# Kernel optimization log

Measured on AMD Instinct MI355X. Metric: run time of the kernel, lower is better.

Reference implementation:

```python
import jax, jax.numpy as jnp
import numpy as np

DIM = 2048
N_HEAD = 32
N_KV = 8
HEAD_DIM = DIM // N_HEAD  # 64
GROUP = N_HEAD // N_KV    # 4


def setup_inputs() -> dict:
    key = jax.random.key(0)
    k1, k2, k3, k4 = jax.random.split(key, 4)
    B, S = 2, 2048
    x = jax.random.normal(k1, (B, S, DIM), dtype=jnp.float32)
    freqs_cis = jax.random.normal(k2, (S, HEAD_DIM // 2, 2), dtype=jnp.float32)
    wqkv_w = jax.random.normal(k3, (DIM, (N_HEAD + 2 * N_KV) * HEAD_DIM), dtype=jnp.float32) * 0.02
    wo_w = jax.random.normal(k4, (DIM, DIM), dtype=jnp.float32) * 0.02
    return {"x": x, "freqs_cis": freqs_cis, "wqkv_w": wqkv_w, "wo_w": wo_w}


def apply_rotary_emb(x, freqs_cis):
    # x: (B, S, H, head_dim), freqs_cis: (S, head_dim//2, 2)
    B, S, H, D = x.shape
    xs = x.astype(jnp.float32).reshape(B, S, H, D // 2, 2)
    fc = freqs_cis.reshape(1, S, 1, D // 2, 2)
    real = xs[..., 0] * fc[..., 0] - xs[..., 1] * fc[..., 1]
    imag = xs[..., 1] * fc[..., 0] + xs[..., 0] * fc[..., 1]
    out = jnp.stack([real, imag], axis=-1).reshape(B, S, H, D)
    return out.astype(x.dtype)


def reference(x, freqs_cis, wqkv_w, wo_w):
    B, S, _ = x.shape
    kv_size = N_KV * HEAD_DIM
    qkv = x @ wqkv_w  # (B, S, (n_head+2*n_kv)*head_dim)
    xq = qkv[..., :DIM].reshape(B, S, N_HEAD, HEAD_DIM)
    xk = qkv[..., DIM:DIM + kv_size].reshape(B, S, N_KV, HEAD_DIM)
    xv = qkv[..., DIM + kv_size:].reshape(B, S, N_KV, HEAD_DIM)

    xq = apply_rotary_emb(xq, freqs_cis)
    xk = apply_rotary_emb(xk, freqs_cis)

    # GQA without materializing repeated KV heads:
    # q: (B, n_kv, group, S, d); k, v: (B, n_kv, S, d)
    q = xq.transpose(0, 2, 1, 3).reshape(B, N_KV, GROUP, S, HEAD_DIM)
    k = xk.transpose(0, 2, 1, 3)
    v = xv.transpose(0, 2, 1, 3)

    scale = 1.0 / jnp.sqrt(jnp.asarray(HEAD_DIM, dtype=q.dtype))
    scores = jnp.einsum('bkgqd,bkKd->bkgqK', q, k) * scale  # (B, n_kv, group, S, S)
    causal = jnp.tril(jnp.ones((S, S), dtype=bool))
    neg = jnp.asarray(jnp.finfo(scores.dtype).min, dtype=scores.dtype)
    scores = jnp.where(causal, scores, neg)
    probs = jax.nn.softmax(scores, axis=-1)
    out = jnp.einsum('bkgqK,bkKd->bkgqd', probs, v)  # (B, n_kv, group, S, d)
    out = out.reshape(B, N_HEAD, S, HEAD_DIM).transpose(0, 2, 1, 3).reshape(B, S, DIM)
    return out @ wo_w
```

## Files before the change

kernel.cpp:

```cpp
#include <hip/hip_runtime.h>
#include <hip/hip_bf16.h>
#include <math.h>

#define DIM 2048
#define NH 32
#define NKV 8
#define HD 64
#define SEQ 2048
#define BATCH 2
#define MTOT (BATCH*SEQ)
#define QKV_N ((NH + 2*NKV)*HD)
#define QSCALE 0.18033688011112042f

typedef __bf16 bf16x8 __attribute__((ext_vector_type(8)));
typedef float f32x4 __attribute__((ext_vector_type(4)));

#if __has_builtin(__builtin_amdgcn_exp2f)
#define EXP2F __builtin_amdgcn_exp2f
#else
#define EXP2F exp2f
#endif

__device__ __forceinline__ void gld_lds16(const void* g, void* l) {
  __builtin_amdgcn_global_load_lds((__attribute__((address_space(1))) void*)g,
                                   (__attribute__((address_space(3))) void*)l,
                                   16, 0, 0);
}

__global__ void cvt_x_kernel(const float* __restrict__ src, __hip_bfloat16* __restrict__ dst, int n4) {
  int i = blockIdx.x * 256 + threadIdx.x;
  if (i >= n4) return;
  float4 v = ((const float4*)src)[i];
  union { __hip_bfloat16 h[4]; uint2 u; } t;
  t.h[0] = __float2bfloat16(v.x); t.h[1] = __float2bfloat16(v.y);
  t.h[2] = __float2bfloat16(v.z); t.h[3] = __float2bfloat16(v.w);
  ((uint2*)dst)[i] = t.u;
}

__global__ void transpose_cvt_kernel(const float* __restrict__ src, __hip_bfloat16* __restrict__ dst,
                                     int R, int C) {
  __shared__ float tile[32][33];
  int c0 = blockIdx.x * 32, r0 = blockIdx.y * 32;
  int tx = threadIdx.x & 31, ty = threadIdx.x >> 5;
  #pragma unroll
  for (int i = ty; i < 32; i += 8)
    tile[i][tx] = src[(size_t)(r0 + i) * C + c0 + tx];
  __syncthreads();
  #pragma unroll
  for (int i = ty; i < 32; i += 8)
    dst[(size_t)(c0 + i) * R + r0 + tx] = __float2bfloat16(tile[tx][i]);
}

__global__ __launch_bounds__(128) void gemm_qkv_rope_kernel(const __hip_bfloat16* __restrict__ A,
                                                            const __hip_bfloat16* __restrict__ Bt,
                                                            const float* __restrict__ freqs,
                                                            __hip_bfloat16* __restrict__ Qb,
                                                            __hip_bfloat16* __restrict__ Kb,
                                                            __hip_bfloat16* __restrict__ Vb) {
  __shared__ __hip_bfloat16 As[64 * 32];
  __shared__ __hip_bfloat16 Bs[128 * 32];
  const int tid = threadIdx.x;
  const int w = tid >> 6, lane = tid & 63, ln = lane & 15, quad = lane >> 4;
  const int id = blockIdx.x;
  const int by = (id & 7) * 8 + ((id >> 3) & 7);
  const int bx = id >> 6;
  const int m0 = by * 64, n0 = bx * 128;
  const int K = DIM;
  const __hip_bfloat16* Ag = A + (size_t)(m0 + w * 32 + (lane >> 2)) * K + (lane & 3) * 8;
  const __hip_bfloat16* Bg = Bt + (size_t)(n0 + w * 64 + (lane >> 2)) * K + (lane & 3) * 8;
  __hip_bfloat16* AsW = &As[w * 1024];
  __hip_bfloat16* BsW = &Bs[w * 2048];
  f32x4 acc[4][4] = {};
  for (int k0 = 0; k0 < K; k0 += 32) {
    gld_lds16(Ag + k0, AsW);
    gld_lds16(Ag + (size_t)16 * K + k0, AsW + 512);
    #pragma unroll
    for (int c = 0; c < 4; c++)
      gld_lds16(Bg + (size_t)(c * 16) * K + k0, BsW + c * 512);
    __syncthreads();
    bf16x8 af[4], bf[4];
    #pragma unroll
    for (int i = 0; i < 4; i++)
      af[i] = *(const bf16x8*)&As[(i * 16 + ln) * 32 + quad * 8];
    #pragma unroll
    for (int j = 0; j < 4; j++)
      bf[j] = *(const bf16x8*)&Bs[(w * 64 + j * 16 + ln) * 32 + quad * 8];
    #pragma unroll
    for (int i = 0; i < 4; i++)
      #pragma unroll
      for (int j = 0; j < 4; j++)
        acc[i][j] = __builtin_amdgcn_mfma_f32_16x16x32_bf16(af[i], bf[j], acc[i][j], 0, 0, 0);
    __syncthreads();
  }
  const int region = (n0 >= 2560) ? 2 : (n0 >= 2048 ? 1 : 0);
  #pragma unroll
  for (int i = 0; i < 4; i++) {
    #pragma unroll
    for (int j = 0; j < 4; j++) {
      const int n = n0 + w * 64 + j * 16 + ln;
      const int d = n & 63;
      #pragma unroll
      for (int r = 0; r < 4; r++) {
        const int m = m0 + i * 16 + quad * 4 + r;
        const int bb = m >> 11, s = m & 2047;
        float v = acc[i][j][r];
        if (region == 2) {
          Vb[((size_t)(bb * NKV + ((n - 2560) >> 6)) * SEQ + s) * HD + d] = __float2bfloat16(v);
        } else {
          float p = __shfl_xor(v, 1);
          const float2 fc = *(const float2*)&freqs[s * 64 + (d & ~1)];
          float o = (d & 1) ? (v * fc.x + p * fc.y) : (v * fc.x - p * fc.y);
          if (region == 0)
            Qb[((size_t)(bb * NH + (n >> 6)) * SEQ + s) * HD + d] = __float2bfloat16(o * QSCALE);
          else
            Kb[((size_t)(bb * NKV + ((n - 2048) >> 6)) * SEQ + s) * HD + d] = __float2bfloat16(o);
        }
      }
    }
  }
}

__global__ __launch_bounds__(128) void gemm_wo_kernel(const __hip_bfloat16* __restrict__ A,
                                                      const __hip_bfloat16* __restrict__ Bt,
                                                      float* __restrict__ C) {
  __shared__ __hip_bfloat16 As[64 * 32];
  __shared__ __hip_bfloat16 Bs[128 * 32];
  const int tid = threadIdx.x;
  const int w = tid >> 6, lane = tid & 63, ln = lane & 15, quad = lane >> 4;
  const int id = blockIdx.x;
  const int by = (id & 7) * 8 + ((id >> 3) & 7);
  const int bx = id >> 6;
  const int m0 = by * 64, n0 = bx * 128;
  const int K = DIM, N = DIM;
  const __hip_bfloat16* Ag = A + (size_t)(m0 + w * 32 + (lane >> 2)) * K + (lane & 3) * 8;
  const __hip_bfloat16* Bg = Bt + (size_t)(n0 + w * 64 + (lane >> 2)) * K + (lane & 3) * 8;
  __hip_bfloat16* AsW = &As[w * 1024];
  __hip_bfloat16* BsW = &Bs[w * 2048];
  f32x4 acc[4][4] = {};
  for (int k0 = 0; k0 < K; k0 += 32) {
    gld_lds16(Ag + k0, AsW);
    gld_lds16(Ag + (size_t)16 * K + k0, AsW + 512);
    #pragma unroll
    for (int c = 0; c < 4; c++)
      gld_lds16(Bg + (size_t)(c * 16) * K + k0, BsW + c * 512);
    __syncthreads();
    bf16x8 af[4], bf[4];
    #pragma unroll
    for (int i = 0; i < 4; i++)
      af[i] = *(const bf16x8*)&As[(i * 16 + ln) * 32 + quad * 8];
    #pragma unroll
    for (int j = 0; j < 4; j++)
      bf[j] = *(const bf16x8*)&Bs[(w * 64 + j * 16 + ln) * 32 + quad * 8];
    #pragma unroll
    for (int i = 0; i < 4; i++)
      #pragma unroll
      for (int j = 0; j < 4; j++)
        acc[i][j] = __builtin_amdgcn_mfma_f32_16x16x32_bf16(af[i], bf[j], acc[i][j], 0, 0, 0);
    __syncthreads();
  }
  #pragma unroll
  for (int i = 0; i < 4; i++) {
    const int r0 = m0 + i * 16 + quad * 4;
    #pragma unroll
    for (int j = 0; j < 4; j++) {
      const int cc = n0 + w * 64 + j * 16 + ln;
      #pragma unroll
      for (int r = 0; r < 4; r++)
        C[(size_t)(r0 + r) * N + cc] = acc[i][j][r];
    }
  }
}

__global__ __launch_bounds__(256, 3) void attn_kernel(const __hip_bfloat16* __restrict__ Q,
                                                      const __hip_bfloat16* __restrict__ Kg,
                                                      const __hip_bfloat16* __restrict__ Vg,
                                                      __hip_bfloat16* __restrict__ O) {
  __shared__ __hip_bfloat16 Ks[128 * 64];
  __shared__ __hip_bfloat16 Vs[64 * 136];
  __shared__ __hip_bfloat16 Ps[4][32 * 72];
  const int id = blockIdx.x;
  const int xcd = id & 7, slot = id >> 3;
  const int cmb = xcd * 2 + (slot >> 6);
  const int b = cmb >> 3, kvh = cmb & 7;
  const int s_ = slot & 63;
  const int t = 15 - (s_ >> 2);
  const int h = kvh * 4 + (s_ & 3);
  const int tid = threadIdx.x, w = tid >> 6, lane = tid & 63, ln = lane & 15, quad = lane >> 4;
  const size_t qbase = (size_t)(b * NH + h) * SEQ * HD;
  const size_t kbase = (size_t)(b * NKV + kvh) * SEQ * HD;

  const __hip_bfloat16* Kgl = Kg + kbase + (size_t)(tid >> 3) * 64 + (size_t)(((tid & 7) ^ ((tid >> 3) & 7)) * 8);
  const int vrow = tid >> 2, vcb = (tid & 3) * 16, vsw = (tid & 3) << 4;
  const int psw = ((ln >> 2) & 3) << 4;

  const int qgw = t * 128 + w * 32;
  bf16x8 qf[2][2];
  #pragma unroll
  for (int f = 0; f < 2; f++)
    #pragma unroll
    for (int kt = 0; kt < 2; kt++)
      qf[f][kt] = *(const bf16x8*)(Q + qbase + (size_t)(qgw + f * 16 + ln) * HD + kt * 32 + quad * 8);
  f32x4 Oacc[2][4] = {};
  float lrow[2][4] = {};
  union { unsigned short u[8]; bf16x8 v; } onesu;
  #pragma unroll
  for (int i = 0; i < 8; i++) onesu.u[i] = 0x3F80;
  const bf16x8 ones = onesu.v;

  uint4 vd[2][2];
  #pragma unroll
  for (int bt = 0; bt < 2; bt++)
    #pragma unroll
    for (int cc = 0; cc < 2; cc++)
      vd[bt][cc] = *(const uint4*)(Vg + kbase + (size_t)(bt * 64 + vrow) * HD + vcb + cc * 8);

  for (int j = 0; j <= t; j++) {
    #pragma unroll
    for (int c = 0; c < 4; c++)
      gld_lds16(Kgl + (size_t)j * 8192 + c * 2048, &Ks[c * 2048 + w * 512]);
    #pragma unroll
    for (int bt = 0; bt < 2; bt++)
      #pragma unroll
      for (int cc = 0; cc < 2; cc++) {
        const __hip_bfloat16* vp = (const __hip_bfloat16*)&vd[bt][cc];
        const int col = vcb + cc * 8;
        const int sr = (bt * 64 + vrow) ^ vsw;
        #pragma unroll
        for (int e = 0; e < 8; e++)
          Vs[(col + e) * 136 + sr] = vp[e];
      }
    __syncthreads();
    if (j < t) {
      #pragma unroll
      for (int bt = 0; bt < 2; bt++)
        #pragma unroll
        for (int cc = 0; cc < 2; cc++)
          vd[bt][cc] = *(const uint4*)(Vg + kbase + (size_t)((j + 1) * 128 + bt * 64 + vrow) * HD + vcb + cc * 8);
    }
    const bool lastIter = (j == t);
    #pragma unroll
    for (int s2 = 0; s2 < 2; s2++) {
      if (lastIter && s2 * 64 > w * 32 + 31) continue;
      bf16x8 kf[4][2];
      #pragma unroll
      for (int nt = 0; nt < 4; nt++)
        #pragma unroll
        for (int kt = 0; kt < 2; kt++) {
          const int kv = s2 * 64 + nt * 16 + ln;
          kf[nt][kt] = *(const bf16x8*)&Ks[(kv * 8 + ((kt * 4 + quad) ^ (ln & 7))) * 8];
        }
      #pragma unroll
      for (int f = 0; f < 2; f++) {
        if (lastIter && s2 * 64 > w * 32 + f * 16 + 15) continue;
        f32x4 sf[4];
        #pragma unroll
        for (int nt = 0; nt < 4; nt++) {
          f32x4 s = {};
          s = __builtin_amdgcn_mfma_f32_16x16x32_bf16(qf[f][0], kf[nt][0], s, 0, 0, 0);
          s = __builtin_amdgcn_mfma_f32_16x16x32_bf16(qf[f][1], kf[nt][1], s, 0, 0, 0);
          sf[nt] = s;
        }
        if (lastIter && s2 * 64 + 63 > w * 32 + f * 16) {
          const int qr = w * 32 + f * 16 + quad * 4;
          #pragma unroll
          for (int nt = 0; nt < 4; nt++) {
            const int kg = s2 * 64 + nt * 16 + ln;
            #pragma unroll
            for (int r = 0; r < 4; r++)
              if (kg > qr + r) sf[nt][r] = -1.0e38f;
          }
        }
        #pragma unroll
        for (int nt = 0; nt < 4; nt++)
          #pragma unroll
          for (int r = 0; r < 4; r++)
            Ps[w][(f * 16 + quad * 4 + r) * 72 + ((nt * 16 + ln) ^ (quad << 4))] =
                __float2bfloat16(EXP2F(sf[nt][r]));
      }
      #pragma unroll
      for (int f = 0; f < 2; f++) {
        if (lastIter && s2 * 64 > w * 32 + f * 16 + 15) continue;
        f32x4 ls = {};
        #pragma unroll
        for (int kt = 0; kt < 2; kt++) {
          bf16x8 pf = *(const bf16x8*)&Ps[w][(f * 16 + ln) * 72 + ((kt * 32 + quad * 8) ^ psw)];
          ls = __builtin_amdgcn_mfma_f32_16x16x32_bf16(pf, ones, ls, 0, 0, 0);
          #pragma unroll
          for (int dt = 0; dt < 4; dt++) {
            bf16x8 vf = *(const bf16x8*)&Vs[(dt * 16 + ln) * 136 + s2 * 64 + ((kt * 32 + quad * 8) ^ (dt << 4))];
            Oacc[f][dt] = __builtin_amdgcn_mfma_f32_16x16x32_bf16(pf, vf, Oacc[f][dt], 0, 0, 0);
          }
        }
        #pragma unroll
        for (int r = 0; r < 4; r++) lrow[f][r] += ls[r];
      }
    }
    __syncthreads();
  }
  #pragma unroll
  for (int f = 0; f < 2; f++) {
    const int so = qgw + f * 16 + quad * 4;
    #pragma unroll
    for (int r = 0; r < 4; r++) {
      const float inv = 1.0f / lrow[f][r];
      #pragma unroll
      for (int dt = 0; dt < 4; dt++)
        O[((size_t)(b * SEQ) + so + r) * DIM + h * HD + dt * 16 + ln] =
            __float2bfloat16(Oacc[f][dt][r] * inv);
    }
  }
}

extern "C" void kernel_launch(void* const* d_in, const int* in_sizes, int n_in,
                              void* d_out, int out_size, void* d_ws, size_t ws_size,
                              hipStream_t stream) {
  const float* x     = (const float*)d_in[0];
  const float* freqs = (const float*)d_in[1];
  const float* wqkv  = (const float*)d_in[2];
  const float* wo    = (const float*)d_in[3];
  float* out = (float*)d_out;

  char* ws = (char*)d_ws;
  __hip_bfloat16* xb    = (__hip_bfloat16*)ws; ws += (size_t)MTOT * DIM * 2;
  __hip_bfloat16* wqkvT = (__hip_bfloat16*)ws; ws += (size_t)QKV_N * DIM * 2;
  __hip_bfloat16* woT   = (__hip_bfloat16*)ws; ws += (size_t)DIM * DIM * 2;
  __hip_bfloat16* Qb    = (__hip_bfloat16*)ws; ws += (size_t)BATCH * NH * SEQ * HD * 2;
  __hip_bfloat16* Kb    = (__hip_bfloat16*)ws; ws += (size_t)BATCH * NKV * SEQ * HD * 2;
  __hip_bfloat16* Vb    = (__hip_bfloat16*)ws; ws += (size_t)BATCH * NKV * SEQ * HD * 2;
  __hip_bfloat16* attnb = (__hip_bfloat16*)ws; ws += (size_t)MTOT * DIM * 2;

  cvt_x_kernel<<<(MTOT * DIM / 4 + 255) / 256, 256, 0, stream>>>(x, xb, MTOT * DIM / 4);
  transpose_cvt_kernel<<<dim3(QKV_N / 32, DIM / 32), 256, 0, stream>>>(wqkv, wqkvT, DIM, QKV_N);
  transpose_cvt_kernel<<<dim3(DIM / 32, DIM / 32), 256, 0, stream>>>(wo, woT, DIM, DIM);
  gemm_qkv_rope_kernel<<<1536, 128, 0, stream>>>(xb, wqkvT, freqs, Qb, Kb, Vb);
  attn_kernel<<<1024, 256, 0, stream>>>(Qb, Kb, Vb, attnb);
  gemm_wo_kernel<<<1024, 128, 0, stream>>>(attnb, woT, out);
}
```

Measured before the change: 368.1 us.

## Enlarge GEMM block tiles to 128x128 with four waves in 2x2 layout

```diff
diff --git a/kernel.cpp b/kernel.cpp
--- a/kernel.cpp
+++ b/kernel.cpp
@@ -51,40 +51,40 @@
     dst[(size_t)(c0 + i) * R + r0 + tx] = __float2bfloat16(tile[tx][i]);
 }
 
-__global__ __launch_bounds__(128) void gemm_qkv_rope_kernel(const __hip_bfloat16* __restrict__ A,
+__global__ __launch_bounds__(256) void gemm_qkv_rope_kernel(const __hip_bfloat16* __restrict__ A,
                                                             const __hip_bfloat16* __restrict__ Bt,
                                                             const float* __restrict__ freqs,
                                                             __hip_bfloat16* __restrict__ Qb,
                                                             __hip_bfloat16* __restrict__ Kb,
                                                             __hip_bfloat16* __restrict__ Vb) {
-  __shared__ __hip_bfloat16 As[64 * 32];
+  __shared__ __hip_bfloat16 As[128 * 32];
   __shared__ __hip_bfloat16 Bs[128 * 32];
   const int tid = threadIdx.x;
   const int w = tid >> 6, lane = tid & 63, ln = lane & 15, quad = lane >> 4;
+  const int wr = w >> 1, wc = w & 1;
   const int id = blockIdx.x;
-  const int by = (id & 7) * 8 + ((id >> 3) & 7);
-  const int bx = id >> 6;
-  const int m0 = by * 64, n0 = bx * 128;
+  const int wg = (id & 7) * 96 + (id >> 3);
+  const int bx = wg % 24, by = wg / 24;
+  const int m0 = by * 128, n0 = bx * 128;
   const int K = DIM;
-  const __hip_bfloat16* Ag = A + (size_t)(m0 + w * 32 + (lane >> 2)) * K + (lane & 3) * 8;
-  const __hip_bfloat16* Bg = Bt + (size_t)(n0 + w * 64 + (lane >> 2)) * K + (lane & 3) * 8;
-  __hip_bfloat16* AsW = &As[w * 1024];
-  __hip_bfloat16* BsW = &Bs[w * 2048];
+  const __hip_bfloat16* Ag = A + (size_t)(m0 + w * 16 + (lane >> 2)) * K + (lane & 3) * 8;
+  const __hip_bfloat16* Bg = Bt + (size_t)(n0 + w * 16 + (lane >> 2)) * K + (lane & 3) * 8;
+  __hip_bfloat16* AsW = &As[w * 512];
+  __hip_bfloat16* BsW = &Bs[w * 512];
   f32x4 acc[4][4] = {};
   for (int k0 = 0; k0 < K; k0 += 32) {
     gld_lds16(Ag + k0, AsW);
-    gld_lds16(Ag + (size_t)16 * K + k0, AsW + 512);
-    #pragma unroll
-    for (int c = 0; c < 4; c++)
-      gld_lds16(Bg + (size_t)(c * 16) * K + k0, BsW + c * 512);
+    gld_lds16(Ag + (size_t)64 * K + k0, AsW + 2048);
+    gld_lds16(Bg + k0, BsW);
+    gld_lds16(Bg + (size_t)64 * K + k0, BsW + 2048);
     __syncthreads();
     bf16x8 af[4], bf[4];
     #pragma unroll
     for (int i = 0; i < 4; i++)
-      af[i] = *(const bf16x8*)&As[(i * 16 + ln) * 32 + quad * 8];
+      af[i] = *(const bf16x8*)&As[(wr * 64 + i * 16 + ln) * 32 + quad * 8];
     #pragma unroll
     for (int j = 0; j < 4; j++)
-      bf[j] = *(const bf16x8*)&Bs[(w * 64 + j * 16 + ln) * 32 + quad * 8];
+      bf[j] = *(const bf16x8*)&Bs[(wc * 64 + j * 16 + ln) * 32 + quad * 8];
     #pragma unroll
     for (int i = 0; i < 4; i++)
       #pragma unroll
@@ -97,11 +97,11 @@
   for (int i = 0; i < 4; i++) {
     #pragma unroll
     for (int j = 0; j < 4; j++) {
-      const int n = n0 + w * 64 + j * 16 + ln;
+      const int n = n0 + wc * 64 + j * 16 + ln;
       const int d = n & 63;
       #pragma unroll
       for (int r = 0; r < 4; r++) {
-        const int m = m0 + i * 16 + quad * 4 + r;
+        const int m = m0 + wr * 64 + i * 16 + quad * 4 + r;
         const int bb = m >> 11, s = m & 2047;
         float v = acc[i][j][r];
         if (region == 2) {
@@ -120,37 +120,37 @@
   }
 }
 
-__global__ __launch_bounds__(128) void gemm_wo_kernel(const __hip_bfloat16* __restrict__ A,
+__global__ __launch_bounds__(256) void gemm_wo_kernel(const __hip_bfloat16* __restrict__ A,
                                                       const __hip_bfloat16* __restrict__ Bt,
                                                       float* __restrict__ C) {
-  __shared__ __hip_bfloat16 As[64 * 32];
+  __shared__ __hip_bfloat16 As[128 * 32];
   __shared__ __hip_bfloat16 Bs[128 * 32];
   const int tid = threadIdx.x;
   const int w = tid >> 6, lane = tid & 63, ln = lane & 15, quad = lane >> 4;
+  const int wr = w >> 1, wc = w & 1;
   const int id = blockIdx.x;
-  const int by = (id & 7) * 8 + ((id >> 3) & 7);
-  const int bx = id >> 6;
-  const int m0 = by * 64, n0 = bx * 128;
+  const int wg = (id & 7) * 64 + (id >> 3);
+  const int bx = wg & 15, by = wg >> 4;
+  const int m0 = by * 128, n0 = bx * 128;
   const int K = DIM, N = DIM;
-  const __hip_bfloat16* Ag = A + (size_t)(m0 + w * 32 + (lane >> 2)) * K + (lane & 3) * 8;
-  const __hip_bfloat16* Bg = Bt + (size_t)(n0 + w * 64 + (lane >> 2)) * K + (lane & 3) * 8;
-  __hip_bfloat16* AsW = &As[w * 1024];
-  __hip_bfloat16* BsW = &Bs[w * 2048];
+  const __hip_bfloat16* Ag = A + (size_t)(m0 + w * 16 + (lane >> 2)) * K + (lane & 3) * 8;
+  const __hip_bfloat16* Bg = Bt + (size_t)(n0 + w * 16 + (lane >> 2)) * K + (lane & 3) * 8;
+  __hip_bfloat16* AsW = &As[w * 512];
+  __hip_bfloat16* BsW = &Bs[w * 512];
   f32x4 acc[4][4] = {};
   for (int k0 = 0; k0 < K; k0 += 32) {
     gld_lds16(Ag + k0, AsW);
-    gld_lds16(Ag + (size_t)16 * K + k0, AsW + 512);
-    #pragma unroll
-    for (int c = 0; c < 4; c++)
-      gld_lds16(Bg + (size_t)(c * 16) * K + k0, BsW + c * 512);
+    gld_lds16(Ag + (size_t)64 * K + k0, AsW + 2048);
+    gld_lds16(Bg + k0, BsW);
+    gld_lds16(Bg + (size_t)64 * K + k0, BsW + 2048);
     __syncthreads();
     bf16x8 af[4], bf[4];
     #pragma unroll
     for (int i = 0; i < 4; i++)
-      af[i] = *(const bf16x8*)&As[(i * 16 + ln) * 32 + quad * 8];
+      af[i] = *(const bf16x8*)&As[(wr * 64 + i * 16 + ln) * 32 + quad * 8];
     #pragma unroll
     for (int j = 0; j < 4; j++)
-      bf[j] = *(const bf16x8*)&Bs[(w * 64 + j * 16 + ln) * 32 + quad * 8];
+      bf[j] = *(const bf16x8*)&Bs[(wc * 64 + j * 16 + ln) * 32 + quad * 8];
     #pragma unroll
     for (int i = 0; i < 4; i++)
       #pragma unroll
@@ -160,10 +160,10 @@
   }
   #pragma unroll
   for (int i = 0; i < 4; i++) {
-    const int r0 = m0 + i * 16 + quad * 4;
+    const int r0 = m0 + wr * 64 + i * 16 + quad * 4;
     #pragma unroll
     for (int j = 0; j < 4; j++) {
-      const int cc = n0 + w * 64 + j * 16 + ln;
+      const int cc = n0 + wc * 64 + j * 16 + ln;
       #pragma unroll
       for (int r = 0; r < 4; r++)
         C[(size_t)(r0 + r) * N + cc] = acc[i][j][r];
@@ -332,7 +332,7 @@
   cvt_x_kernel<<<(MTOT * DIM / 4 + 255) / 256, 256, 0, stream>>>(x, xb, MTOT * DIM / 4);
   transpose_cvt_kernel<<<dim3(QKV_N / 32, DIM / 32), 256, 0, stream>>>(wqkv, wqkvT, DIM, QKV_N);
   transpose_cvt_kernel<<<dim3(DIM / 32, DIM / 32), 256, 0, stream>>>(wo, woT, DIM, DIM);
-  gemm_qkv_rope_kernel<<<1536, 128, 0, stream>>>(xb, wqkvT, freqs, Qb, Kb, Vb);
+  gemm_qkv_rope_kernel<<<768, 256, 0, stream>>>(xb, wqkvT, freqs, Qb, Kb, Vb);
   attn_kernel<<<1024, 256, 0, stream>>>(Qb, Kb, Vb, attnb);
-  gemm_wo_kernel<<<1024, 128, 0, stream>>>(attnb, woT, out);
-}
+  gemm_wo_kernel<<<512, 256, 0, stream>>>(attnb, woT, out);
+}
```

Result: no change. 373.2 us (+1.4%).
